# Optimization experiments

Hardware: AMD Instinct MI355X
Metric: run time of the kernel (lower is better)

The kernel has to match this reference:

```python
import jax, jax.numpy as jnp
import numpy as np

N = 65536          # pixels
F = 224            # spectral bands (num_features)
P = 6              # num_endmembers
H = 256            # hidden_dim


def setup_inputs() -> dict:
    key = jax.random.key(0)
    ks = jax.random.split(key, 8)
    s = lambda fan_in: 1.0 / np.sqrt(fan_in)
    return {
        "abundance_matrix": jax.random.normal(ks[0], (N, P), jnp.float32),
        "Y": jax.random.normal(ks[1], (N, F), jnp.float32),
        "W1": jax.random.normal(ks[2], (F, H), jnp.float32) * s(F),
        "b1": jnp.zeros((H,), jnp.float32),
        "W2": jax.random.normal(ks[3], (H, H), jnp.float32) * s(H),
        "b2": jnp.zeros((H,), jnp.float32),
        "W3": jax.random.normal(ks[4], (H, F), jnp.float32) * s(H),
        "b3": jnp.zeros((F,), jnp.float32),
    }


def reference(abundance_matrix, Y, W1, b1, W2, b2, W3, b3):
    # MLP is pointwise over pixels, so apply once to all pixels [N,F] -> [N,F]
    h = jax.nn.relu(Y @ W1 + b1)
    h = jax.nn.relu(h @ W2 + b2)
    logits = h @ W3 + b3                      # [N, F]

    cls = jnp.argmax(abundance_matrix, axis=-1)          # [N]
    masks = cls[None, :] == jnp.arange(P)[:, None]       # [P, N]

    # Masked per-class softmax over the pixel axis (per feature column).
    neg = jnp.finfo(logits.dtype).min
    masked_logits = jnp.where(masks[:, :, None], logits[None], neg)  # [P, N, F]
    w = jax.nn.softmax(masked_logits, axis=1)                        # [P, N, F]
    w = w * masks[:, :, None]                                        # exact zeros off-class

    M = jnp.einsum('pnf,nf->pf', w, Y)                   # [P, F] endmembers
    counts = masks.sum(axis=1)                           # [P]
    M = jnp.where((counts > 0)[:, None], M, jnp.zeros_like(M))

    Y_hat = abundance_matrix @ M                         # [N, F]
    return Y_hat
```

## Files before the change

### kernel.cpp

```cpp
#include <hip/hip_runtime.h>
#include <stdint.h>

typedef short s16x8 __attribute__((ext_vector_type(8)));
typedef short s16x4 __attribute__((ext_vector_type(4)));
typedef float f32x4 __attribute__((ext_vector_type(4)));

#define NPIX 65536
#define FEAT 224
#define PEND 6
#define HID  256

__device__ __forceinline__ unsigned short f2bf(float x) {
  unsigned u = __float_as_uint(x);
  return (unsigned short)((u + 0x7FFFu + ((u >> 16) & 1u)) >> 16);
}
__device__ __forceinline__ float bf2f(unsigned short b) {
  return __uint_as_float(((unsigned)b) << 16);
}
__device__ __forceinline__ void glds16(const void* g, void* l) {
  __builtin_amdgcn_global_load_lds(
      (const __attribute__((address_space(1))) unsigned int*)g,
      (__attribute__((address_space(3))) unsigned int*)l, 16, 0, 0);
}

#define WAITV(n) asm volatile("s_waitcnt vmcnt(" #n ")" ::: "memory")
#define BAR_LGKM() asm volatile("s_waitcnt lgkmcnt(0)\ns_barrier" ::: "memory")

__global__ void cvtW_all(const float* __restrict__ W1, const float* __restrict__ W2,
                         const float* __restrict__ W3,
                         unsigned short* __restrict__ W1t, unsigned short* __restrict__ W2t,
                         unsigned short* __restrict__ W3t, float* __restrict__ gz) {
  int i = blockIdx.x * 256 + threadIdx.x;
  if (i < 57344) {
    int n = i / 224, k = i - n * 224;
    W1t[i] = f2bf(W1[k * 256 + n]);
  } else if (i < 122880) {
    int i2 = i - 57344;
    int n = i2 >> 8, k = i2 & 255;
    W2t[i2] = f2bf(W2[k * 256 + n]);
  } else if (i < 188416) {
    int i3 = i - 122880;
    int n = i3 >> 8, k = i3 & 255;
    W3t[i3] = (n < FEAT) ? f2bf(W3[k * FEAT + n]) : (unsigned short)0;
  } else if (i < 191104) {
    gz[i - 188416] = 0.f;
  }
}

__global__ __launch_bounds__(256, 2)
void fused_mlp(const float* __restrict__ Y,
               const unsigned short* __restrict__ W1t,
               const unsigned short* __restrict__ W2t,
               const unsigned short* __restrict__ W3t,
               const float* __restrict__ b1, const float* __restrict__ b2,
               const float* __restrict__ b3, const float* __restrict__ ab,
               float* __restrict__ gsum, float* __restrict__ gsumY) {
  __shared__ __align__(16) unsigned short hS[64 * 256];
  __shared__ __align__(16) unsigned short Bs[2][8192];
  unsigned short* AsB = hS;
  float* redE = (float*)&Bs[0][0];
  float* redY = redE + PEND * FEAT;
  unsigned short* clsS = (unsigned short*)(redY + PEND * FEAT);

  const int tid = threadIdx.x;
  const int wid = tid >> 6, lane = tid & 63;
  const int mrow = lane & 15, quad = lane >> 4;
  const int brow = lane >> 2, bk8 = (lane & 3) * 8;
  const int arow = tid >> 2, aqtr = tid & 3;
  const long row0 = (long)blockIdx.x * 64;

  f32x4 acc[4][4];
  float4 pv0, pv1;

#define STAGE_W(s) do {                                                     \
    const unsigned short* Wp_; int ld_, k0_;                                \
    if ((s) < 7)       { Wp_ = W1t; ld_ = 224; k0_ = (s) * 32; }            \
    else if ((s) < 15) { Wp_ = W2t; ld_ = 256; k0_ = ((s) - 7) * 32; }      \
    else               { Wp_ = W3t; ld_ = 256; k0_ = ((s) - 15) * 32; }     \
    unsigned short* dst_ = &Bs[(s) & 1][wid * 2048];                        \
    _Pragma("unroll")                                                       \
    for (int c_ = 0; c_ < 4; c_++)                                          \
      glds16(Wp_ + (wid * 64 + c_ * 16 + brow) * ld_ + k0_ + bk8,           \
             dst_ + c_ * 512);                                              \
  } while (0)

#define LOADA(p) do {                                                       \
    const float* s_ = Y + (row0 + arow) * FEAT + (p) * 32 + aqtr * 8;       \
    pv0 = *(const float4*)s_; pv1 = *(const float4*)(s_ + 4);               \
  } while (0)

#define WRITEA(p) do {                                                      \
    unsigned short* d_ = AsB + ((p) & 1) * 2304 + arow * 36 + aqtr * 8;     \
    s16x4 lo_ = {(short)f2bf(pv0.x), (short)f2bf(pv0.y),                    \
                 (short)f2bf(pv0.z), (short)f2bf(pv0.w)};                   \
    s16x4 hi_ = {(short)f2bf(pv1.x), (short)f2bf(pv1.y),                    \
                 (short)f2bf(pv1.z), (short)f2bf(pv1.w)};                   \
    *(s16x4*)d_ = lo_; *(s16x4*)(d_ + 4) = hi_;                             \
  } while (0)

#define LOAD_B(buf)                                                         \
    _Pragma("unroll")                                                       \
    for (int j = 0; j < 4; j++)                                             \
      bfv[j] = *(const s16x8*)(&Bs[buf][(wid * 64 + j * 16 + mrow) * 32 + quad * 8]);

#define MFMA_ALL() do {                                                     \
    __builtin_amdgcn_s_setprio(1);                                          \
    _Pragma("unroll")                                                       \
    for (int i = 0; i < 4; i++)                                             \
      _Pragma("unroll")                                                     \
      for (int j = 0; j < 4; j++)                                           \
        acc[i][j] = __builtin_amdgcn_mfma_f32_16x16x32_bf16(af[i], bfv[j], acc[i][j], 0, 0, 0); \
    __builtin_amdgcn_s_setprio(0);                                          \
  } while (0)

#define ZERO_ACC()                                                          \
    _Pragma("unroll")                                                       \
    for (int i = 0; i < 4; i++)                                             \
      _Pragma("unroll")                                                     \
      for (int j = 0; j < 4; j++) acc[i][j] = {0.f, 0.f, 0.f, 0.f};

  ZERO_ACC();
  LOADA(0); STAGE_W(0); WRITEA(0);
  __syncthreads();
  for (int p = 0; p < 7; p++) {
    if (p < 6) { LOADA(p + 1); STAGE_W(p + 1); WAITV(6); }
    else       { STAGE_W(7);   WAITV(4); }
    s16x8 af[4], bfv[4];
    const unsigned short* Ab = AsB + (p & 1) * 2304;
#pragma unroll
    for (int i = 0; i < 4; i++) {
      const unsigned short* pa = Ab + (i * 16 + mrow) * 36 + quad * 8;
      s16x4 lo = *(const s16x4*)pa, hi = *(const s16x4*)(pa + 4);
      af[i] = __builtin_shufflevector(lo, hi, 0, 1, 2, 3, 4, 5, 6, 7);
    }
    LOAD_B(p & 1);
    MFMA_ALL();
    if (p < 6) WRITEA(p + 1);
    BAR_LGKM();
  }
#pragma unroll
  for (int j = 0; j < 4; j++) {
    int col = wid * 64 + j * 16 + mrow;
    float bb = b1[col];
    int cs = col >> 3, c7 = col & 7;
#pragma unroll
    for (int i = 0; i < 4; i++) {
#pragma unroll
      for (int r = 0; r < 4; r++) {
        int row = i * 16 + quad * 4 + r;
        hS[row * 256 + ((cs ^ (row & 7)) << 3) + c7] = f2bf(fmaxf(acc[i][j][r] + bb, 0.f));
      }
    }
  }
  BAR_LGKM();

  ZERO_ACC();
  for (int p = 0; p < 8; p++) {
    STAGE_W(8 + p);
    WAITV(4);
    const int k0 = p * 32;
    s16x8 af[4], bfv[4];
#pragma unroll
    for (int i = 0; i < 4; i++) {
      int R = i * 16 + mrow;
      int ch = (k0 >> 3) + quad;
      af[i] = *(const s16x8*)(hS + R * 256 + ((ch ^ (R & 7)) << 3));
    }
    LOAD_B((7 + p) & 1);
    MFMA_ALL();
  }
  BAR_LGKM();
#pragma unroll
  for (int j = 0; j < 4; j++) {
    int col = wid * 64 + j * 16 + mrow;
    float bb = b2[col];
    int cs = col >> 3, c7 = col & 7;
#pragma unroll
    for (int i = 0; i < 4; i++) {
#pragma unroll
      for (int r = 0; r < 4; r++) {
        int row = i * 16 + quad * 4 + r;
        hS[row * 256 + ((cs ^ (row & 7)) << 3) + c7] = f2bf(fmaxf(acc[i][j][r] + bb, 0.f));
      }
    }
  }
  BAR_LGKM();

  ZERO_ACC();
  for (int p = 0; p < 8; p++) {
    if (p < 7) { STAGE_W(16 + p); WAITV(4); }
    else       { WAITV(0); }
    const int k0 = p * 32;
    s16x8 af[4], bfv[4];
#pragma unroll
    for (int i = 0; i < 4; i++) {
      int R = i * 16 + mrow;
      int ch = (k0 >> 3) + quad;
      af[i] = *(const s16x8*)(hS + R * 256 + ((ch ^ (R & 7)) << 3));
    }
    LOAD_B((15 + p) & 1);
    MFMA_ALL();
  }
  BAR_LGKM();

#pragma unroll
  for (int j = 0; j < 4; j++) {
    int col = wid * 64 + j * 16 + mrow;
    if (col < FEAT) {
      float bb = b3[col];
      int cs = col >> 3, c7 = col & 7;
#pragma unroll
      for (int i = 0; i < 4; i++) {
#pragma unroll
        for (int r = 0; r < 4; r++) {
          int row = i * 16 + quad * 4 + r;
          hS[row * 256 + ((cs ^ (row & 7)) << 3) + c7] = f2bf(__expf(acc[i][j][r] + bb));
        }
      }
    }
  }
  if (tid < 64) {
    const float* a = ab + (row0 + tid) * PEND;
    float best = a[0]; int c = 0;
#pragma unroll
    for (int p = 1; p < PEND; p++) { float v = a[p]; if (v > best) { best = v; c = p; } }
    clsS[tid] = (unsigned short)c;
  }
  BAR_LGKM();

  const bool act = lane < 56;
  const int f0 = lane * 4;
  float accE[PEND][4], accY[PEND][4];
#pragma unroll
  for (int p = 0; p < PEND; p++)
#pragma unroll
    for (int i = 0; i < 4; i++) { accE[p][i] = 0.f; accY[p][i] = 0.f; }

#pragma unroll 4
  for (int r = wid; r < 64; r += 4) {
    int c = __builtin_amdgcn_readfirstlane((int)clsS[r]);
    if (act) {
      const unsigned short* pe = hS + r * 256 + (((f0 >> 3) ^ (r & 7)) << 3) + (f0 & 7);
      ushort4 e4 = *(const ushort4*)pe;
      float4 y4 = *(const float4*)(Y + (row0 + r) * FEAT + f0);
      float e[4] = {bf2f(e4.x), bf2f(e4.y), bf2f(e4.z), bf2f(e4.w)};
      float ey[4] = {e[0] * y4.x, e[1] * y4.y, e[2] * y4.z, e[3] * y4.w};
#define RK_CASE(P)                                                               \
      case P:                                                                    \
        _Pragma("unroll")                                                        \
        for (int i = 0; i < 4; i++) { accE[P][i] += e[i]; accY[P][i] += ey[i]; } \
        break;
      switch (c) {
        RK_CASE(0) RK_CASE(1) RK_CASE(2) RK_CASE(3) RK_CASE(4) RK_CASE(5)
      }
#undef RK_CASE
    }
  }

  for (int w = 0; w < 4; w++) {
    if (wid == w && act) {
#pragma unroll
      for (int p = 0; p < PEND; p++) {
        float4* pe = (float4*)(redE + p * FEAT + f0);
        float4* py = (float4*)(redY + p * FEAT + f0);
        float4 ve = {accE[p][0], accE[p][1], accE[p][2], accE[p][3]};
        float4 vy = {accY[p][0], accY[p][1], accY[p][2], accY[p][3]};
        if (w == 0) { *pe = ve; *py = vy; }
        else {
          float4 oe = *pe, oy = *py;
          oe.x += ve.x; oe.y += ve.y; oe.z += ve.z; oe.w += ve.w;
          oy.x += vy.x; oy.y += vy.y; oy.z += vy.z; oy.w += vy.w;
          *pe = oe; *py = oy;
        }
      }
    }
    __syncthreads();
  }

  for (int i = tid; i < PEND * FEAT; i += 256) {
    atomicAdd(&gsum[i], redE[i]);
    atomicAdd(&gsumY[i], redY[i]);
  }
#undef STAGE_W
#undef LOADA
#undef WRITEA
#undef LOAD_B
#undef MFMA_ALL
#undef ZERO_ACC
}

__global__ __launch_bounds__(256)
void yhat(const float* __restrict__ ab, const float* __restrict__ gsum,
          const float* __restrict__ gsumY, float* __restrict__ out) {
  constexpr int ROWS = 64;
  __shared__ float Ms[PEND * FEAT];
  __shared__ float aS[ROWS * PEND];
  const int tid = threadIdx.x;
  for (int i = tid; i < PEND * FEAT; i += 256) {
    float s = gsum[i];
    Ms[i] = (s > 0.f) ? gsumY[i] / s : 0.f;
  }
  const long n0 = (long)blockIdx.x * ROWS;
  for (int i = tid; i < ROWS * PEND; i += 256) aS[i] = ab[n0 * PEND + i];
  __syncthreads();

  const int wid = tid >> 6;
  const int lane = tid & 63;
  if (lane >= 56) return;
  const int f0 = lane * 4;
  float4 Mr[PEND];
#pragma unroll
  for (int p = 0; p < PEND; p++) Mr[p] = *(const float4*)(Ms + p * FEAT + f0);

  for (int r = wid; r < ROWS; r += 4) {
    float a[PEND];
#pragma unroll
    for (int p = 0; p < PEND; p++) a[p] = aS[r * PEND + p];
    float4 o = {0.f, 0.f, 0.f, 0.f};
#pragma unroll
    for (int p = 0; p < PEND; p++) {
      o.x += a[p] * Mr[p].x; o.y += a[p] * Mr[p].y;
      o.z += a[p] * Mr[p].z; o.w += a[p] * Mr[p].w;
    }
    *(float4*)(out + (n0 + r) * FEAT + f0) = o;
  }
}

extern "C" void kernel_launch(void* const* d_in, const int* in_sizes, int n_in,
                              void* d_out, int out_size, void* d_ws, size_t ws_size,
                              hipStream_t stream) {
  const float* ab = (const float*)d_in[0];
  const float* Y  = (const float*)d_in[1];
  const float* W1 = (const float*)d_in[2];
  const float* b1 = (const float*)d_in[3];
  const float* W2 = (const float*)d_in[4];
  const float* b2 = (const float*)d_in[5];
  const float* W3 = (const float*)d_in[6];
  const float* b3 = (const float*)d_in[7];
  float* out = (float*)d_out;

  char* ws = (char*)d_ws;
  const size_t oW1t  = 0;
  const size_t oW2t  = 114688;
  const size_t oW3t  = 245760;
  const size_t osum  = 376832;

  unsigned short* W1t = (unsigned short*)(ws + oW1t);
  unsigned short* W2t = (unsigned short*)(ws + oW2t);
  unsigned short* W3t = (unsigned short*)(ws + oW3t);
  float* gsum  = (float*)(ws + osum);
  float* gsumY = (float*)(ws + osum + 5376);

  cvtW_all<<<747, 256, 0, stream>>>(W1, W2, W3, W1t, W2t, W3t, gsum);
  fused_mlp<<<1024, 256, 0, stream>>>(Y, W1t, W2t, W3t, b1, b2, b3, ab, gsum, gsumY);
  yhat<<<1024, 256, 0, stream>>>(ab, gsum, gsumY, out);
}
```

Measured before the change: 201.1 us.

## Load MLP weight fragments directly to registers instead of staging through LDS

Weight B-fragments are now loaded from global memory straight into registers with a one-step register double buffer, replacing the global_load_lds staging into a double-buffered shared buffer. This removes that shared buffer, so the reduction scratch gets its own smaller arrays, and occupancy is raised to 3 blocks per CU through launch bounds. The k-loops are fully unrolled and the MFMA priority hints are dropped. The cost is more register pressure and global/L2 weight traffic per wave, with less latency hiding, since each wave fetches its own fragments and relies on the compiler's waitcnt placement.

```diff
diff --git a/kernel.cpp b/kernel.cpp
--- a/kernel.cpp
+++ b/kernel.cpp
@@ -17,13 +17,7 @@
 __device__ __forceinline__ float bf2f(unsigned short b) {
   return __uint_as_float(((unsigned)b) << 16);
 }
-__device__ __forceinline__ void glds16(const void* g, void* l) {
-  __builtin_amdgcn_global_load_lds(
-      (const __attribute__((address_space(1))) unsigned int*)g,
-      (__attribute__((address_space(3))) unsigned int*)l, 16, 0, 0);
-}
-
-#define WAITV(n) asm volatile("s_waitcnt vmcnt(" #n ")" ::: "memory")
+
 #define BAR_LGKM() asm volatile("s_waitcnt lgkmcnt(0)\ns_barrier" ::: "memory")
 
 __global__ void cvtW_all(const float* __restrict__ W1, const float* __restrict__ W2,
@@ -47,7 +41,7 @@
   }
 }
 
-__global__ __launch_bounds__(256, 2)
+__global__ __launch_bounds__(256, 3)
 void fused_mlp(const float* __restrict__ Y,
                const unsigned short* __restrict__ W1t,
                const unsigned short* __restrict__ W2t,
@@ -56,32 +50,30 @@
                const float* __restrict__ b3, const float* __restrict__ ab,
                float* __restrict__ gsum, float* __restrict__ gsumY) {
   __shared__ __align__(16) unsigned short hS[64 * 256];
-  __shared__ __align__(16) unsigned short Bs[2][8192];
+  __shared__ __align__(16) float redE[PEND * FEAT];
+  __shared__ __align__(16) float redY[PEND * FEAT];
+  __shared__ __align__(16) unsigned short clsS[64];
   unsigned short* AsB = hS;
-  float* redE = (float*)&Bs[0][0];
-  float* redY = redE + PEND * FEAT;
-  unsigned short* clsS = (unsigned short*)(redY + PEND * FEAT);
 
   const int tid = threadIdx.x;
   const int wid = tid >> 6, lane = tid & 63;
   const int mrow = lane & 15, quad = lane >> 4;
-  const int brow = lane >> 2, bk8 = (lane & 3) * 8;
   const int arow = tid >> 2, aqtr = tid & 3;
   const long row0 = (long)blockIdx.x * 64;
 
   f32x4 acc[4][4];
+  s16x8 bcur[4];
   float4 pv0, pv1;
 
-#define STAGE_W(s) do {                                                     \
+#define LOADB_G(dst, s) do {                                                \
     const unsigned short* Wp_; int ld_, k0_;                                \
     if ((s) < 7)       { Wp_ = W1t; ld_ = 224; k0_ = (s) * 32; }            \
     else if ((s) < 15) { Wp_ = W2t; ld_ = 256; k0_ = ((s) - 7) * 32; }      \
     else               { Wp_ = W3t; ld_ = 256; k0_ = ((s) - 15) * 32; }     \
-    unsigned short* dst_ = &Bs[(s) & 1][wid * 2048];                        \
     _Pragma("unroll")                                                       \
-    for (int c_ = 0; c_ < 4; c_++)                                          \
-      glds16(Wp_ + (wid * 64 + c_ * 16 + brow) * ld_ + k0_ + bk8,           \
-             dst_ + c_ * 512);                                              \
+    for (int j_ = 0; j_ < 4; j_++)                                          \
+      dst[j_] = *(const s16x8*)(Wp_ +                                       \
+          (size_t)(wid * 64 + j_ * 16 + mrow) * ld_ + k0_ + quad * 8);      \
   } while (0)
 
 #define LOADA(p) do {                                                       \
@@ -98,20 +90,12 @@
     *(s16x4*)d_ = lo_; *(s16x4*)(d_ + 4) = hi_;                             \
   } while (0)
 
-#define LOAD_B(buf)                                                         \
-    _Pragma("unroll")                                                       \
-    for (int j = 0; j < 4; j++)                                             \
-      bfv[j] = *(const s16x8*)(&Bs[buf][(wid * 64 + j * 16 + mrow) * 32 + quad * 8]);
-
-#define MFMA_ALL() do {                                                     \
-    __builtin_amdgcn_s_setprio(1);                                          \
+#define MFMA_ALL()                                                          \
     _Pragma("unroll")                                                       \
     for (int i = 0; i < 4; i++)                                             \
       _Pragma("unroll")                                                     \
       for (int j = 0; j < 4; j++)                                           \
-        acc[i][j] = __builtin_amdgcn_mfma_f32_16x16x32_bf16(af[i], bfv[j], acc[i][j], 0, 0, 0); \
-    __builtin_amdgcn_s_setprio(0);                                          \
-  } while (0)
+        acc[i][j] = __builtin_amdgcn_mfma_f32_16x16x32_bf16(af[i], bcur[j], acc[i][j], 0, 0, 0);
 
 #define ZERO_ACC()                                                          \
     _Pragma("unroll")                                                       \
@@ -119,13 +103,21 @@
       _Pragma("unroll")                                                     \
       for (int j = 0; j < 4; j++) acc[i][j] = {0.f, 0.f, 0.f, 0.f};
 
+#define BSWAP()                                                             \
+    _Pragma("unroll")                                                       \
+    for (int j_ = 0; j_ < 4; j_++) bcur[j_] = bnxt[j_];
+
   ZERO_ACC();
-  LOADA(0); STAGE_W(0); WRITEA(0);
-  __syncthreads();
+  LOADA(0);
+  LOADB_G(bcur, 0);
+  WRITEA(0);
+  BAR_LGKM();
+#pragma unroll
   for (int p = 0; p < 7; p++) {
-    if (p < 6) { LOADA(p + 1); STAGE_W(p + 1); WAITV(6); }
-    else       { STAGE_W(7);   WAITV(4); }
-    s16x8 af[4], bfv[4];
+    s16x8 bnxt[4];
+    if (p < 6) { LOADA(p + 1); LOADB_G(bnxt, p + 1); }
+    else       { LOADB_G(bnxt, 7); }
+    s16x8 af[4];
     const unsigned short* Ab = AsB + (p & 1) * 2304;
 #pragma unroll
     for (int i = 0; i < 4; i++) {
@@ -133,10 +125,10 @@
       s16x4 lo = *(const s16x4*)pa, hi = *(const s16x4*)(pa + 4);
       af[i] = __builtin_shufflevector(lo, hi, 0, 1, 2, 3, 4, 5, 6, 7);
     }
-    LOAD_B(p & 1);
     MFMA_ALL();
     if (p < 6) WRITEA(p + 1);
     BAR_LGKM();
+    BSWAP();
   }
 #pragma unroll
   for (int j = 0; j < 4; j++) {
@@ -155,19 +147,20 @@
   BAR_LGKM();
 
   ZERO_ACC();
+#pragma unroll
   for (int p = 0; p < 8; p++) {
-    STAGE_W(8 + p);
-    WAITV(4);
+    s16x8 bnxt[4];
+    LOADB_G(bnxt, 8 + p);
     const int k0 = p * 32;
-    s16x8 af[4], bfv[4];
+    s16x8 af[4];
 #pragma unroll
     for (int i = 0; i < 4; i++) {
       int R = i * 16 + mrow;
       int ch = (k0 >> 3) + quad;
       af[i] = *(const s16x8*)(hS + R * 256 + ((ch ^ (R & 7)) << 3));
     }
-    LOAD_B((7 + p) & 1);
     MFMA_ALL();
+    BSWAP();
   }
   BAR_LGKM();
 #pragma unroll
@@ -187,19 +180,20 @@
   BAR_LGKM();
 
   ZERO_ACC();
+#pragma unroll
   for (int p = 0; p < 8; p++) {
-    if (p < 7) { STAGE_W(16 + p); WAITV(4); }
-    else       { WAITV(0); }
+    s16x8 bnxt[4];
+    if (p < 7) LOADB_G(bnxt, 16 + p);
     const int k0 = p * 32;
-    s16x8 af[4], bfv[4];
+    s16x8 af[4];
 #pragma unroll
     for (int i = 0; i < 4; i++) {
       int R = i * 16 + mrow;
       int ch = (k0 >> 3) + quad;
       af[i] = *(const s16x8*)(hS + R * 256 + ((ch ^ (R & 7)) << 3));
     }
-    LOAD_B((15 + p) & 1);
     MFMA_ALL();
+    if (p < 7) BSWAP();
   }
   BAR_LGKM();
 
@@ -281,12 +275,12 @@
     atomicAdd(&gsum[i], redE[i]);
     atomicAdd(&gsumY[i], redY[i]);
   }
-#undef STAGE_W
+#undef LOADB_G
 #undef LOADA
 #undef WRITEA
-#undef LOAD_B
 #undef MFMA_ALL
 #undef ZERO_ACC
+#undef BSWAP
 }
 
 __global__ __launch_bounds__(256)
```

Measured after the change: 248.2 us. 23.5% more time.

## Replace hand-coded waitcnt barriers with __syncthreads and raise occupancy to three blocks

Applied to the files above, without the earlier changes.

The hand-written vmcnt waits and the combined lgkmcnt/barrier asm are replaced by plain __syncthreads. A barrier is now added at the end of every K-step in the second and third GEMM loops, which closes a possible race on the double-buffered weight tiles. MFMA priority bumping is removed. The reduction scratch moves from the weight buffer into the hidden buffer, and the class array gets its own shared array. Launch bounds go from two to three blocks per CU to raise occupancy. The compiler-generated barrier likely waits on all outstanding loads, including the async prefetch just issued, so it risks losing load/compute overlap and adding register pressure or spills.

```diff
diff --git a/kernel.cpp b/kernel.cpp
--- a/kernel.cpp
+++ b/kernel.cpp
@@ -22,9 +22,6 @@
       (const __attribute__((address_space(1))) unsigned int*)g,
       (__attribute__((address_space(3))) unsigned int*)l, 16, 0, 0);
 }
-
-#define WAITV(n) asm volatile("s_waitcnt vmcnt(" #n ")" ::: "memory")
-#define BAR_LGKM() asm volatile("s_waitcnt lgkmcnt(0)\ns_barrier" ::: "memory")
 
 __global__ void cvtW_all(const float* __restrict__ W1, const float* __restrict__ W2,
                          const float* __restrict__ W3,
@@ -47,7 +44,7 @@
   }
 }
 
-__global__ __launch_bounds__(256, 2)
+__global__ __launch_bounds__(256, 3)
 void fused_mlp(const float* __restrict__ Y,
                const unsigned short* __restrict__ W1t,
                const unsigned short* __restrict__ W2t,
@@ -57,10 +54,10 @@
                float* __restrict__ gsum, float* __restrict__ gsumY) {
   __shared__ __align__(16) unsigned short hS[64 * 256];
   __shared__ __align__(16) unsigned short Bs[2][8192];
+  __shared__ __align__(16) unsigned short clsS[64];
   unsigned short* AsB = hS;
-  float* redE = (float*)&Bs[0][0];
+  float* redE = (float*)hS;
   float* redY = redE + PEND * FEAT;
-  unsigned short* clsS = (unsigned short*)(redY + PEND * FEAT);
 
   const int tid = threadIdx.x;
   const int wid = tid >> 6, lane = tid & 63;
@@ -80,7 +77,7 @@
     unsigned short* dst_ = &Bs[(s) & 1][wid * 2048];                        \
     _Pragma("unroll")                                                       \
     for (int c_ = 0; c_ < 4; c_++)                                          \
-      glds16(Wp_ + (wid * 64 + c_ * 16 + brow) * ld_ + k0_ + bk8,           \
+      glds16(Wp_ + (size_t)(wid * 64 + c_ * 16 + brow) * ld_ + k0_ + bk8,   \
              dst_ + c_ * 512);                                              \
   } while (0)
 
@@ -103,15 +100,12 @@
     for (int j = 0; j < 4; j++)                                             \
       bfv[j] = *(const s16x8*)(&Bs[buf][(wid * 64 + j * 16 + mrow) * 32 + quad * 8]);
 
-#define MFMA_ALL() do {                                                     \
-    __builtin_amdgcn_s_setprio(1);                                          \
+#define MFMA_ALL()                                                          \
     _Pragma("unroll")                                                       \
     for (int i = 0; i < 4; i++)                                             \
       _Pragma("unroll")                                                     \
       for (int j = 0; j < 4; j++)                                           \
-        acc[i][j] = __builtin_amdgcn_mfma_f32_16x16x32_bf16(af[i], bfv[j], acc[i][j], 0, 0, 0); \
-    __builtin_amdgcn_s_setprio(0);                                          \
-  } while (0)
+        acc[i][j] = __builtin_amdgcn_mfma_f32_16x16x32_bf16(af[i], bfv[j], acc[i][j], 0, 0, 0);
 
 #define ZERO_ACC()                                                          \
     _Pragma("unroll")                                                       \
@@ -123,8 +117,8 @@
   LOADA(0); STAGE_W(0); WRITEA(0);
   __syncthreads();
   for (int p = 0; p < 7; p++) {
-    if (p < 6) { LOADA(p + 1); STAGE_W(p + 1); WAITV(6); }
-    else       { STAGE_W(7);   WAITV(4); }
+    if (p < 6) { LOADA(p + 1); STAGE_W(p + 1); }
+    else       { STAGE_W(7); }
     s16x8 af[4], bfv[4];
     const unsigned short* Ab = AsB + (p & 1) * 2304;
 #pragma unroll
@@ -136,7 +130,7 @@
     LOAD_B(p & 1);
     MFMA_ALL();
     if (p < 6) WRITEA(p + 1);
-    BAR_LGKM();
+    __syncthreads();
   }
 #pragma unroll
   for (int j = 0; j < 4; j++) {
@@ -152,13 +146,12 @@
       }
     }
   }
-  BAR_LGKM();
+  __syncthreads();
 
   ZERO_ACC();
   for (int p = 0; p < 8; p++) {
-    STAGE_W(8 + p);
-    WAITV(4);
-    const int k0 = p * 32;
+    STAGE_W(p < 7 ? 8 + p : 15);
+    const int k0 = p * 32, buf = (7 + p) & 1;
     s16x8 af[4], bfv[4];
 #pragma unroll
     for (int i = 0; i < 4; i++) {
@@ -166,10 +159,10 @@
       int ch = (k0 >> 3) + quad;
       af[i] = *(const s16x8*)(hS + R * 256 + ((ch ^ (R & 7)) << 3));
     }
-    LOAD_B((7 + p) & 1);
+    LOAD_B(buf);
     MFMA_ALL();
-  }
-  BAR_LGKM();
+    __syncthreads();
+  }
 #pragma unroll
   for (int j = 0; j < 4; j++) {
     int col = wid * 64 + j * 16 + mrow;
@@ -184,13 +177,12 @@
       }
     }
   }
-  BAR_LGKM();
+  __syncthreads();
 
   ZERO_ACC();
   for (int p = 0; p < 8; p++) {
-    if (p < 7) { STAGE_W(16 + p); WAITV(4); }
-    else       { WAITV(0); }
-    const int k0 = p * 32;
+    if (p < 7) STAGE_W(16 + p);
+    const int k0 = p * 32, buf = (15 + p) & 1;
     s16x8 af[4], bfv[4];
 #pragma unroll
     for (int i = 0; i < 4; i++) {
@@ -198,11 +190,10 @@
       int ch = (k0 >> 3) + quad;
       af[i] = *(const s16x8*)(hS + R * 256 + ((ch ^ (R & 7)) << 3));
     }
-    LOAD_B((15 + p) & 1);
+    LOAD_B(buf);
     MFMA_ALL();
-  }
-  BAR_LGKM();
-
+    __syncthreads();
+  }
 #pragma unroll
   for (int j = 0; j < 4; j++) {
     int col = wid * 64 + j * 16 + mrow;
@@ -226,7 +217,7 @@
     for (int p = 1; p < PEND; p++) { float v = a[p]; if (v > best) { best = v; c = p; } }
     clsS[tid] = (unsigned short)c;
   }
-  BAR_LGKM();
+  __syncthreads();
 
   const bool act = lane < 56;
   const int f0 = lane * 4;
@@ -256,6 +247,7 @@
 #undef RK_CASE
     }
   }
+  __syncthreads();
 
   for (int w = 0; w < 4; w++) {
     if (wid == w && act) {
```

Measured after the change: 206.4 us. +2.6%, slower.
